# Kernel optimization log

Measured on AMD Instinct MI355X. Metric: run time of the kernel, lower is better.

## Reference

```python
import jax, jax.numpy as jnp
import numpy as np

GROUP = 128  # per-group quantization along the input dimension


def _quantize_int4(w):
    """Asymmetric INT4 per-group quantization. w: [out, in] -> (q, scale, zero).
    q: int32 in [0,15], shape [out, in//GROUP, GROUP]; scale/zero: [out, in//GROUP]."""
    o, i = w.shape
    wg = w.reshape(o, i // GROUP, GROUP)
    mn = wg.min(axis=-1)
    mx = wg.max(axis=-1)
    scale = (mx - mn) / 15.0
    scale = jnp.where(scale == 0, jnp.float32(1.0), scale)
    zero = jnp.clip(jnp.round(-mn / scale), 0.0, 15.0)
    q = jnp.clip(jnp.round(wg / scale[..., None]) + zero[..., None], 0.0, 15.0).astype(jnp.int32)
    return q, scale.astype(jnp.float32), zero.astype(jnp.float32)


def _dequant(q, s, z):
    """(q - zero) * scale, regrouped back to [out, in]."""
    w = (q.astype(jnp.float32) - z[..., None]) * s[..., None]
    return w.reshape(q.shape[0], -1)


def setup_inputs() -> dict:
    key = jax.random.key(0)
    ks = jax.random.split(key, 5)
    B, D_IN, D_H, D_OUT = 512, 2048, 8192, 2048
    x = jax.random.normal(ks[0], (B, D_IN), dtype=jnp.float32)
    w1 = jax.random.normal(ks[1], (D_H, D_IN), dtype=jnp.float32) * 0.02
    b1 = jax.random.normal(ks[2], (D_H,), dtype=jnp.float32) * 0.01
    w2 = jax.random.normal(ks[3], (D_OUT, D_H), dtype=jnp.float32) * 0.02
    b2 = jax.random.normal(ks[4], (D_OUT,), dtype=jnp.float32) * 0.01
    q1, s1, z1 = _quantize_int4(w1)
    q2, s2, z2 = _quantize_int4(w2)
    return {"x": x, "q1": q1, "s1": s1, "z1": z1, "b1": b1,
            "q2": q2, "s2": s2, "z2": z2, "b2": b2}


def reference(x, q1, s1, z1, b1, q2, s2, z2, b2):
    # Layer 1: INT4 dequant + Linear + ReLU (fused in the native kernel)
    w1 = _dequant(q1, s1, z1)              # [D_H, D_IN]
    h = jax.nn.relu(x @ w1.T + b1)         # [B, D_H]
    # Layer 2: INT4 dequant + Linear (no activation)
    w2 = _dequant(q2, s2, z2)              # [D_OUT, D_H]
    return h @ w2.T + b2                   # [B, D_OUT]
```

## Files before the change

### kernel.cpp

```cpp
#include <hip/hip_runtime.h>
#include <stdint.h>

typedef unsigned short u16;
typedef __attribute__((ext_vector_type(8))) short bf16x8;
typedef __attribute__((ext_vector_type(8))) unsigned short u16x8;
typedef __attribute__((ext_vector_type(4))) float f32x4;
typedef __attribute__((ext_vector_type(4))) int i32x4;

__device__ __forceinline__ u16 f2bf(float f) {
  uint32_t u = __builtin_bit_cast(uint32_t, f);
  u += 0x7fffu + ((u >> 16) & 1u);
  return (u16)(u >> 16);
}

#define GLD16(g, l)                                                         \
  __builtin_amdgcn_global_load_lds(                                         \
      (const __attribute__((address_space(1))) void*)(g),                   \
      (__attribute__((address_space(3))) void*)(l), 16, 0, 0)


__global__ __launch_bounds__(256) void cvt_f32_bf16(const float* __restrict__ src,
                                                    u16* __restrict__ dst, int n8) {
  int t = blockIdx.x * 256 + threadIdx.x;
  if (t >= n8) return;
  f32x4 a = ((const f32x4*)src)[2 * t];
  f32x4 b = ((const f32x4*)src)[2 * t + 1];
  u16x8 o;
  o[0] = f2bf(a[0]); o[1] = f2bf(a[1]); o[2] = f2bf(a[2]); o[3] = f2bf(a[3]);
  o[4] = f2bf(b[0]); o[5] = f2bf(b[1]); o[6] = f2bf(b[2]); o[7] = f2bf(b[3]);
  ((u16x8*)dst)[t] = o;
}

__global__ __launch_bounds__(256) void dequant_w2x(const int* __restrict__ qa,
                                                   const float* __restrict__ sa,
                                                   const float* __restrict__ za,
                                                   u16* __restrict__ wa,
                                                   const int* __restrict__ qb,
                                                   const float* __restrict__ sb,
                                                   const float* __restrict__ zb,
                                                   u16* __restrict__ wb, int n8) {
  int t = blockIdx.x * 256 + threadIdx.x;
  if (t >= n8) return;
  const int* q = blockIdx.z ? qb : qa;
  const float* s = blockIdx.z ? sb : sa;
  const float* z = blockIdx.z ? zb : za;
  u16* w = blockIdx.z ? wb : wa;
  int g = t >> 4;
  float sc = s[g];
  float zp = z[g];
  i32x4 a = ((const i32x4*)q)[2 * t];
  i32x4 b = ((const i32x4*)q)[2 * t + 1];
  u16x8 o;
  o[0] = f2bf(((float)a[0] - zp) * sc);
  o[1] = f2bf(((float)a[1] - zp) * sc);
  o[2] = f2bf(((float)a[2] - zp) * sc);
  o[3] = f2bf(((float)a[3] - zp) * sc);
  o[4] = f2bf(((float)b[0] - zp) * sc);
  o[5] = f2bf(((float)b[1] - zp) * sc);
  o[6] = f2bf(((float)b[2] - zp) * sc);
  o[7] = f2bf(((float)b[3] - zp) * sc);
  ((u16x8*)w)[t] = o;
}

__global__ __launch_bounds__(256) void bias_init(float* __restrict__ out,
                                                 const float* __restrict__ b,
                                                 int N, int n4) {
  int t = blockIdx.x * 256 + threadIdx.x;
  if (t >= n4) return;
  int idx = t * 4;
  int n = idx & (N - 1);
  *(f32x4*)(out + idx) = *(const f32x4*)(b + n);
}

template <bool RELU, bool OUT_BF16, bool ATOMIC>
__global__ __launch_bounds__(256) void gemm_bt(const u16* __restrict__ A,
                                               const u16* __restrict__ Bm,
                                               const float* __restrict__ bias,
                                               void* __restrict__ Cout,
                                               int M, int N, int K, int kChunk) {
  __shared__ u16 As[2][128 * 64];
  __shared__ u16 Bs[2][128 * 64];
  const int tid = threadIdx.x;
  const int wave = tid >> 6;
  const int lane = tid & 63;
  const int m0 = blockIdx.y << 7;
  const int n0 = blockIdx.x << 7;
  const int kStart = blockIdx.z * kChunk;
  const int srow = lane >> 3;
  const int schunk = (((lane & 7) ^ (srow & 7)) << 3);
  const int wm = (wave >> 1) << 6;
  const int wn = (wave & 1) << 6;
  const int quad = lane >> 4;
  const int l15 = lane & 15;
  const int x7 = lane & 7;
  const int c0 = ((quad ^ x7) << 3);
  const int c1 = (((4 | quad) ^ x7) << 3);

  const u16* Ab = A + (size_t)(m0 + 32 * wave + srow) * K + kStart + schunk;
  const u16* Bb = Bm + (size_t)(n0 + 32 * wave + srow) * K + kStart + schunk;
  const int ldsW = (32 * wave) * 64;
  const size_t rs8 = (size_t)8 * K;
  const int nT = kChunk >> 6;

  f32x4 acc[4][4];
#pragma unroll
  for (int i = 0; i < 4; i++)
#pragma unroll
    for (int j = 0; j < 4; j++) acc[i][j] = (f32x4){0.f, 0.f, 0.f, 0.f};

#define STAGE(bi_, t_)                                          \
  do {                                                          \
    const int ko_ = (t_) << 6;                                  \
    GLD16(Ab + ko_,           &As[bi_][ldsW]);                  \
    GLD16(Ab + ko_ + rs8,     &As[bi_][ldsW + 512]);            \
    GLD16(Ab + ko_ + 2 * rs8, &As[bi_][ldsW + 1024]);           \
    GLD16(Ab + ko_ + 3 * rs8, &As[bi_][ldsW + 1536]);           \
    GLD16(Bb + ko_,           &Bs[bi_][ldsW]);                  \
    GLD16(Bb + ko_ + rs8,     &Bs[bi_][ldsW + 512]);            \
    GLD16(Bb + ko_ + 2 * rs8, &Bs[bi_][ldsW + 1024]);           \
    GLD16(Bb + ko_ + 3 * rs8, &Bs[bi_][ldsW + 1536]);           \
  } while (0)

  bf16x8 af0[4], bf0[4], af1[4], bf1[4];
#define LOADFRAGS(bi_)                                                          \
  do {                                                                          \
    _Pragma("unroll") for (int i = 0; i < 4; i++)                               \
        af0[i] = *(const bf16x8*)&As[bi_][(wm + i * 16 + l15) * 64 + c0];       \
    _Pragma("unroll") for (int j = 0; j < 4; j++)                               \
        bf0[j] = *(const bf16x8*)&Bs[bi_][(wn + j * 16 + l15) * 64 + c0];       \
    _Pragma("unroll") for (int i = 0; i < 4; i++)                               \
        af1[i] = *(const bf16x8*)&As[bi_][(wm + i * 16 + l15) * 64 + c1];       \
    _Pragma("unroll") for (int j = 0; j < 4; j++)                               \
        bf1[j] = *(const bf16x8*)&Bs[bi_][(wn + j * 16 + l15) * 64 + c1];       \
  } while (0)

#define MFMA_S0()                                                               \
  do {                                                                          \
    _Pragma("unroll") for (int i = 0; i < 4; i++)                               \
        _Pragma("unroll") for (int j = 0; j < 4; j++)                           \
            acc[i][j] = __builtin_amdgcn_mfma_f32_16x16x32_bf16(                \
                af0[i], bf0[j], acc[i][j], 0, 0, 0);                            \
  } while (0)

#define MFMA_S1()                                                               \
  do {                                                                          \
    _Pragma("unroll") for (int i = 0; i < 4; i++)                               \
        _Pragma("unroll") for (int j = 0; j < 4; j++)                           \
            acc[i][j] = __builtin_amdgcn_mfma_f32_16x16x32_bf16(                \
                af1[i], bf1[j], acc[i][j], 0, 0, 0);                            \
  } while (0)

  STAGE(0, 0);
  STAGE(1, 1);

  int bi = 0;
  for (int t = 0; t < nT - 2; ++t) {
    asm volatile("s_waitcnt vmcnt(8)" ::: "memory");
    __builtin_amdgcn_s_barrier();
    LOADFRAGS(bi);
    asm volatile("s_waitcnt lgkmcnt(8)" ::: "memory");
    __builtin_amdgcn_sched_barrier(0);
    MFMA_S0();
    asm volatile("s_waitcnt lgkmcnt(0)" ::: "memory");
    __builtin_amdgcn_sched_barrier(0);
    __builtin_amdgcn_s_barrier();
    STAGE(bi, t + 2);
    MFMA_S1();
    bi ^= 1;
  }
  asm volatile("s_waitcnt vmcnt(8)" ::: "memory");
  __builtin_amdgcn_s_barrier();
  LOADFRAGS(bi);
  asm volatile("s_waitcnt lgkmcnt(8)" ::: "memory");
  __builtin_amdgcn_sched_barrier(0);
  MFMA_S0();
  asm volatile("s_waitcnt lgkmcnt(0)" ::: "memory");
  __builtin_amdgcn_sched_barrier(0);
  MFMA_S1();
  bi ^= 1;
  asm volatile("s_waitcnt vmcnt(0)" ::: "memory");
  __builtin_amdgcn_s_barrier();
  LOADFRAGS(bi);
  asm volatile("s_waitcnt lgkmcnt(8)" ::: "memory");
  __builtin_amdgcn_sched_barrier(0);
  MFMA_S0();
  asm volatile("s_waitcnt lgkmcnt(0)" ::: "memory");
  __builtin_amdgcn_sched_barrier(0);
  MFMA_S1();

#undef STAGE
#undef LOADFRAGS
#undef MFMA_S0
#undef MFMA_S1

#pragma unroll
  for (int i = 0; i < 4; i++) {
#pragma unroll
    for (int j = 0; j < 4; j++) {
      const int col = n0 + wn + j * 16 + l15;
      float bv = 0.f;
      if (!ATOMIC) bv = bias[col];
#pragma unroll
      for (int r = 0; r < 4; r++) {
        const int row = m0 + wm + i * 16 + quad * 4 + r;
        float v = acc[i][j][r];
        if (ATOMIC) {
          atomicAdd((float*)Cout + (size_t)row * N + col, v);
        } else {
          v += bv;
          if (RELU) v = v > 0.f ? v : 0.f;
          if (OUT_BF16)
            ((u16*)Cout)[(size_t)row * N + col] = f2bf(v);
          else
            ((float*)Cout)[(size_t)row * N + col] = v;
        }
      }
    }
  }
}


extern "C" void kernel_launch(void* const* d_in, const int* in_sizes, int n_in,
                              void* d_out, int out_size, void* d_ws, size_t ws_size,
                              hipStream_t stream) {
  const float* x  = (const float*)d_in[0];
  const int*   q1 = (const int*)d_in[1];
  const float* s1 = (const float*)d_in[2];
  const float* z1 = (const float*)d_in[3];
  const float* b1 = (const float*)d_in[4];
  const int*   q2 = (const int*)d_in[5];
  const float* s2 = (const float*)d_in[6];
  const float* z2 = (const float*)d_in[7];
  const float* b2 = (const float*)d_in[8];
  float* out = (float*)d_out;

  const int B = 512, D_IN = 2048, D_H = 8192, D_OUT = 2048;

  char* ws = (char*)d_ws;
  u16* xb  = (u16*)(ws);
  u16* w1b = (u16*)(ws + (size_t)2 * 1024 * 1024);
  u16* hb  = (u16*)(ws + (size_t)34 * 1024 * 1024);
  u16* w2b = (u16*)(ws + (size_t)42 * 1024 * 1024);

  cvt_f32_bf16<<<(B * D_IN / 8 + 255) / 256, 256, 0, stream>>>(x, xb, B * D_IN / 8);
  {
    const int n8 = D_H * D_IN / 8;
    dim3 gd((n8 + 255) / 256, 1, 2);
    dequant_w2x<<<gd, 256, 0, stream>>>(q1, s1, z1, w1b, q2, s2, z2, w2b, n8);
  }
  dim3 g1(D_H / 128, B / 128, 1);
  gemm_bt<true, true, false><<<g1, 256, 0, stream>>>(xb, w1b, b1, hb, B, D_H, D_IN, D_IN);
  bias_init<<<(B * D_OUT / 4 + 255) / 256, 256, 0, stream>>>(out, b2, D_OUT, B * D_OUT / 4);
  dim3 g2(D_OUT / 128, B / 128, 8);
  gemm_bt<false, false, true><<<g2, 256, 0, stream>>>(hb, w2b, nullptr, out, B, D_OUT, D_H, D_H / 8);
}
```

Measured before the change: 244.2 us.

## Fuse all stages into one persistent kernel with grid-wide barriers

Replaces the five separate launches (convert, dequant, GEMM1, bias init, split-K GEMM2) with a single persistent kernel of 256 blocks. Blocks do the elementwise stages with grid-stride loops, then synchronize through atomic-counter grid barriers before each GEMM phase. This removes launch gaps and inter-kernel idle time, but adds a memset plus spin-wait barriers. It also relies on all 256 blocks being co-resident, and GEMM2 has only one block per work item.

```diff
diff --git a/kernel.cpp b/kernel.cpp
--- a/kernel.cpp
+++ b/kernel.cpp
@@ -2,6 +2,7 @@
 #include <stdint.h>
 
 typedef unsigned short u16;
+typedef unsigned int u32;
 typedef __attribute__((ext_vector_type(8))) short bf16x8;
 typedef __attribute__((ext_vector_type(8))) unsigned short u16x8;
 typedef __attribute__((ext_vector_type(4))) float f32x4;
@@ -18,33 +19,21 @@
       (const __attribute__((address_space(1))) void*)(g),                   \
       (__attribute__((address_space(3))) void*)(l), 16, 0, 0)
 
-
-__global__ __launch_bounds__(256) void cvt_f32_bf16(const float* __restrict__ src,
-                                                    u16* __restrict__ dst, int n8) {
-  int t = blockIdx.x * 256 + threadIdx.x;
-  if (t >= n8) return;
-  f32x4 a = ((const f32x4*)src)[2 * t];
-  f32x4 b = ((const f32x4*)src)[2 * t + 1];
-  u16x8 o;
-  o[0] = f2bf(a[0]); o[1] = f2bf(a[1]); o[2] = f2bf(a[2]); o[3] = f2bf(a[3]);
-  o[4] = f2bf(b[0]); o[5] = f2bf(b[1]); o[6] = f2bf(b[2]); o[7] = f2bf(b[3]);
-  ((u16x8*)dst)[t] = o;
-}
-
-__global__ __launch_bounds__(256) void dequant_w2x(const int* __restrict__ qa,
-                                                   const float* __restrict__ sa,
-                                                   const float* __restrict__ za,
-                                                   u16* __restrict__ wa,
-                                                   const int* __restrict__ qb,
-                                                   const float* __restrict__ sb,
-                                                   const float* __restrict__ zb,
-                                                   u16* __restrict__ wb, int n8) {
-  int t = blockIdx.x * 256 + threadIdx.x;
-  if (t >= n8) return;
-  const int* q = blockIdx.z ? qb : qa;
-  const float* s = blockIdx.z ? sb : sa;
-  const float* z = blockIdx.z ? zb : za;
-  u16* w = blockIdx.z ? wb : wa;
+__device__ __forceinline__ void grid_barrier(u32* ctr, u32 nb) {
+  __syncthreads();
+  if (threadIdx.x == 0) {
+    __threadfence();
+    u32 old = atomicAdd(ctr, 1u);
+    if (old + 1u < nb) {
+      while (atomicAdd(ctr, 0u) < nb) __builtin_amdgcn_s_sleep(2);
+    }
+    __threadfence();
+  }
+  __syncthreads();
+}
+
+__device__ __forceinline__ void deq8(const int* __restrict__ q, const float* __restrict__ s,
+                                     const float* __restrict__ z, u16* __restrict__ w, int t) {
   int g = t >> 4;
   float sc = s[g];
   float zp = z[g];
@@ -62,30 +51,17 @@
   ((u16x8*)w)[t] = o;
 }
 
-__global__ __launch_bounds__(256) void bias_init(float* __restrict__ out,
-                                                 const float* __restrict__ b,
-                                                 int N, int n4) {
-  int t = blockIdx.x * 256 + threadIdx.x;
-  if (t >= n4) return;
-  int idx = t * 4;
-  int n = idx & (N - 1);
-  *(f32x4*)(out + idx) = *(const f32x4*)(b + n);
-}
-
 template <bool RELU, bool OUT_BF16, bool ATOMIC>
-__global__ __launch_bounds__(256) void gemm_bt(const u16* __restrict__ A,
-                                               const u16* __restrict__ Bm,
-                                               const float* __restrict__ bias,
-                                               void* __restrict__ Cout,
-                                               int M, int N, int K, int kChunk) {
-  __shared__ u16 As[2][128 * 64];
-  __shared__ u16 Bs[2][128 * 64];
+__device__ __forceinline__ void gemm_phase(const u16* __restrict__ A,
+                                           const u16* __restrict__ Bm,
+                                           const float* __restrict__ bias,
+                                           void* __restrict__ Cout,
+                                           int N, int K, int kChunk,
+                                           int m0, int n0, int kStart,
+                                           u16* As, u16* Bs) {
   const int tid = threadIdx.x;
   const int wave = tid >> 6;
   const int lane = tid & 63;
-  const int m0 = blockIdx.y << 7;
-  const int n0 = blockIdx.x << 7;
-  const int kStart = blockIdx.z * kChunk;
   const int srow = lane >> 3;
   const int schunk = (((lane & 7) ^ (srow & 7)) << 3);
   const int wm = (wave >> 1) << 6;
@@ -108,30 +84,30 @@
 #pragma unroll
     for (int j = 0; j < 4; j++) acc[i][j] = (f32x4){0.f, 0.f, 0.f, 0.f};
 
-#define STAGE(bi_, t_)                                          \
-  do {                                                          \
-    const int ko_ = (t_) << 6;                                  \
-    GLD16(Ab + ko_,           &As[bi_][ldsW]);                  \
-    GLD16(Ab + ko_ + rs8,     &As[bi_][ldsW + 512]);            \
-    GLD16(Ab + ko_ + 2 * rs8, &As[bi_][ldsW + 1024]);           \
-    GLD16(Ab + ko_ + 3 * rs8, &As[bi_][ldsW + 1536]);           \
-    GLD16(Bb + ko_,           &Bs[bi_][ldsW]);                  \
-    GLD16(Bb + ko_ + rs8,     &Bs[bi_][ldsW + 512]);            \
-    GLD16(Bb + ko_ + 2 * rs8, &Bs[bi_][ldsW + 1024]);           \
-    GLD16(Bb + ko_ + 3 * rs8, &Bs[bi_][ldsW + 1536]);           \
+#define STAGE(bi_, t_)                                                \
+  do {                                                                \
+    const int ko_ = (t_) << 6;                                        \
+    GLD16(Ab + ko_,           As + (bi_) * 8192 + ldsW);              \
+    GLD16(Ab + ko_ + rs8,     As + (bi_) * 8192 + ldsW + 512);        \
+    GLD16(Ab + ko_ + 2 * rs8, As + (bi_) * 8192 + ldsW + 1024);       \
+    GLD16(Ab + ko_ + 3 * rs8, As + (bi_) * 8192 + ldsW + 1536);       \
+    GLD16(Bb + ko_,           Bs + (bi_) * 8192 + ldsW);              \
+    GLD16(Bb + ko_ + rs8,     Bs + (bi_) * 8192 + ldsW + 512);        \
+    GLD16(Bb + ko_ + 2 * rs8, Bs + (bi_) * 8192 + ldsW + 1024);       \
+    GLD16(Bb + ko_ + 3 * rs8, Bs + (bi_) * 8192 + ldsW + 1536);       \
   } while (0)
 
   bf16x8 af0[4], bf0[4], af1[4], bf1[4];
-#define LOADFRAGS(bi_)                                                          \
-  do {                                                                          \
-    _Pragma("unroll") for (int i = 0; i < 4; i++)                               \
-        af0[i] = *(const bf16x8*)&As[bi_][(wm + i * 16 + l15) * 64 + c0];       \
-    _Pragma("unroll") for (int j = 0; j < 4; j++)                               \
-        bf0[j] = *(const bf16x8*)&Bs[bi_][(wn + j * 16 + l15) * 64 + c0];       \
-    _Pragma("unroll") for (int i = 0; i < 4; i++)                               \
-        af1[i] = *(const bf16x8*)&As[bi_][(wm + i * 16 + l15) * 64 + c1];       \
-    _Pragma("unroll") for (int j = 0; j < 4; j++)                               \
-        bf1[j] = *(const bf16x8*)&Bs[bi_][(wn + j * 16 + l15) * 64 + c1];       \
+#define LOADFRAGS(bi_)                                                               \
+  do {                                                                               \
+    _Pragma("unroll") for (int i = 0; i < 4; i++)                                    \
+        af0[i] = *(const bf16x8*)&As[(bi_) * 8192 + (wm + i * 16 + l15) * 64 + c0];  \
+    _Pragma("unroll") for (int j = 0; j < 4; j++)                                    \
+        bf0[j] = *(const bf16x8*)&Bs[(bi_) * 8192 + (wn + j * 16 + l15) * 64 + c0];  \
+    _Pragma("unroll") for (int i = 0; i < 4; i++)                                    \
+        af1[i] = *(const bf16x8*)&As[(bi_) * 8192 + (wm + i * 16 + l15) * 64 + c1];  \
+    _Pragma("unroll") for (int j = 0; j < 4; j++)                                    \
+        bf1[j] = *(const bf16x8*)&Bs[(bi_) * 8192 + (wn + j * 16 + l15) * 64 + c1];  \
   } while (0)
 
 #define MFMA_S0()                                                               \
@@ -219,6 +195,52 @@
   }
 }
 
+__global__ __launch_bounds__(256) void fused_all(
+    const float* __restrict__ x,
+    const int* __restrict__ q1, const float* __restrict__ s1, const float* __restrict__ z1,
+    const float* __restrict__ b1,
+    const int* __restrict__ q2, const float* __restrict__ s2, const float* __restrict__ z2,
+    const float* __restrict__ b2,
+    float* __restrict__ out,
+    u16* __restrict__ xb, u16* __restrict__ w1b, u16* __restrict__ hb, u16* __restrict__ w2b,
+    u32* bars) {
+  __shared__ u16 As[2 * 128 * 64];
+  __shared__ u16 Bs[2 * 128 * 64];
+
+  const int gstride = 256 * 256;
+  const int base = blockIdx.x * 256 + threadIdx.x;
+
+  for (int t = base; t < 131072; t += gstride) {
+    f32x4 a = ((const f32x4*)x)[2 * t];
+    f32x4 b = ((const f32x4*)x)[2 * t + 1];
+    u16x8 o;
+    o[0] = f2bf(a[0]); o[1] = f2bf(a[1]); o[2] = f2bf(a[2]); o[3] = f2bf(a[3]);
+    o[4] = f2bf(b[0]); o[5] = f2bf(b[1]); o[6] = f2bf(b[2]); o[7] = f2bf(b[3]);
+    ((u16x8*)xb)[t] = o;
+  }
+  for (int t = base; t < 2097152; t += gstride) deq8(q1, s1, z1, w1b, t);
+  for (int t = base; t < 2097152; t += gstride) deq8(q2, s2, z2, w2b, t);
+  for (int t = base; t < 262144; t += gstride) {
+    ((f32x4*)out)[t] = *(const f32x4*)(b2 + ((t * 4) & 2047));
+  }
+
+  grid_barrier(bars + 0, gridDim.x);
+
+  gemm_phase<true, true, false>(xb, w1b, b1, hb,
+                                8192, 2048, 2048,
+                                (blockIdx.x >> 6) << 7,
+                                (blockIdx.x & 63) << 7,
+                                0, As, Bs);
+
+  grid_barrier(bars + 1, gridDim.x);
+
+  gemm_phase<false, false, true>(hb, w2b, nullptr, out,
+                                 2048, 8192, 2048,
+                                 ((blockIdx.x >> 4) & 3) << 7,
+                                 (blockIdx.x & 15) << 7,
+                                 (blockIdx.x >> 6) << 11, As, Bs);
+}
+
 
 extern "C" void kernel_launch(void* const* d_in, const int* in_sizes, int n_in,
                               void* d_out, int out_size, void* d_ws, size_t ws_size,
@@ -234,23 +256,15 @@
   const float* b2 = (const float*)d_in[8];
   float* out = (float*)d_out;
 
-  const int B = 512, D_IN = 2048, D_H = 8192, D_OUT = 2048;
-
   char* ws = (char*)d_ws;
   u16* xb  = (u16*)(ws);
   u16* w1b = (u16*)(ws + (size_t)2 * 1024 * 1024);
   u16* hb  = (u16*)(ws + (size_t)34 * 1024 * 1024);
   u16* w2b = (u16*)(ws + (size_t)42 * 1024 * 1024);
-
-  cvt_f32_bf16<<<(B * D_IN / 8 + 255) / 256, 256, 0, stream>>>(x, xb, B * D_IN / 8);
-  {
-    const int n8 = D_H * D_IN / 8;
-    dim3 gd((n8 + 255) / 256, 1, 2);
-    dequant_w2x<<<gd, 256, 0, stream>>>(q1, s1, z1, w1b, q2, s2, z2, w2b, n8);
-  }
-  dim3 g1(D_H / 128, B / 128, 1);
-  gemm_bt<true, true, false><<<g1, 256, 0, stream>>>(xb, w1b, b1, hb, B, D_H, D_IN, D_IN);
-  bias_init<<<(B * D_OUT / 4 + 255) / 256, 256, 0, stream>>>(out, b2, D_OUT, B * D_OUT / 4);
-  dim3 g2(D_OUT / 128, B / 128, 8);
-  gemm_bt<false, false, true><<<g2, 256, 0, stream>>>(hb, w2b, nullptr, out, B, D_OUT, D_H, D_H / 8);
-}
+  u32* bars = (u32*)(ws + (size_t)74 * 1024 * 1024);
+
+  hipMemsetAsync(bars, 0, 2 * sizeof(u32), stream);
+
+  fused_all<<<256, 256, 0, stream>>>(x, q1, s1, z1, b1, q2, s2, z2, b2,
+                                     out, xb, w1b, hb, w2b, bars);
+}
```

Result: slower. 288.3 us (+18.1%).

## Fuse INT4 dequantization into GEMM B-tile staging, drop separate dequant pass

Applied to the files above, without the earlier changes.

Removes the standalone dequant kernel that wrote bf16 copies of both weight matrices. Each GEMM now loads the int32 quantized weights into registers, converts them with scale and zero to bf16, and writes them into swizzled LDS, interleaved with the MFMA pipeline. This avoids writing and then re-reading the bf16 weights in global memory. In exchange each tile reads int32 weights, twice the bytes of bf16, and adds conversion ALU work and register pressure. Since the 128-column weight tiles are re-dequantized by each of the 4 M-block rows, global weight traffic may not shrink much.

```diff
diff --git a/kernel.cpp b/kernel.cpp
--- a/kernel.cpp
+++ b/kernel.cpp
@@ -2,6 +2,7 @@
 #include <stdint.h>
 
 typedef unsigned short u16;
+typedef unsigned int u32;
 typedef __attribute__((ext_vector_type(8))) short bf16x8;
 typedef __attribute__((ext_vector_type(8))) unsigned short u16x8;
 typedef __attribute__((ext_vector_type(4))) float f32x4;
@@ -31,37 +32,6 @@
   ((u16x8*)dst)[t] = o;
 }
 
-__global__ __launch_bounds__(256) void dequant_w2x(const int* __restrict__ qa,
-                                                   const float* __restrict__ sa,
-                                                   const float* __restrict__ za,
-                                                   u16* __restrict__ wa,
-                                                   const int* __restrict__ qb,
-                                                   const float* __restrict__ sb,
-                                                   const float* __restrict__ zb,
-                                                   u16* __restrict__ wb, int n8) {
-  int t = blockIdx.x * 256 + threadIdx.x;
-  if (t >= n8) return;
-  const int* q = blockIdx.z ? qb : qa;
-  const float* s = blockIdx.z ? sb : sa;
-  const float* z = blockIdx.z ? zb : za;
-  u16* w = blockIdx.z ? wb : wa;
-  int g = t >> 4;
-  float sc = s[g];
-  float zp = z[g];
-  i32x4 a = ((const i32x4*)q)[2 * t];
-  i32x4 b = ((const i32x4*)q)[2 * t + 1];
-  u16x8 o;
-  o[0] = f2bf(((float)a[0] - zp) * sc);
-  o[1] = f2bf(((float)a[1] - zp) * sc);
-  o[2] = f2bf(((float)a[2] - zp) * sc);
-  o[3] = f2bf(((float)a[3] - zp) * sc);
-  o[4] = f2bf(((float)b[0] - zp) * sc);
-  o[5] = f2bf(((float)b[1] - zp) * sc);
-  o[6] = f2bf(((float)b[2] - zp) * sc);
-  o[7] = f2bf(((float)b[3] - zp) * sc);
-  ((u16x8*)w)[t] = o;
-}
-
 __global__ __launch_bounds__(256) void bias_init(float* __restrict__ out,
                                                  const float* __restrict__ b,
                                                  int N, int n4) {
@@ -73,11 +43,13 @@
 }
 
 template <bool RELU, bool OUT_BF16, bool ATOMIC>
-__global__ __launch_bounds__(256) void gemm_bt(const u16* __restrict__ A,
-                                               const u16* __restrict__ Bm,
-                                               const float* __restrict__ bias,
-                                               void* __restrict__ Cout,
-                                               int M, int N, int K, int kChunk) {
+__global__ __launch_bounds__(256, 2) void gemm_dq(const u16* __restrict__ A,
+                                                  const int* __restrict__ Q,
+                                                  const float* __restrict__ S,
+                                                  const float* __restrict__ Z,
+                                                  const float* __restrict__ bias,
+                                                  void* __restrict__ Cout,
+                                                  int N, int K, int kChunk) {
   __shared__ u16 As[2][128 * 64];
   __shared__ u16 Bs[2][128 * 64];
   const int tid = threadIdx.x;
@@ -86,8 +58,20 @@
   const int m0 = blockIdx.y << 7;
   const int n0 = blockIdx.x << 7;
   const int kStart = blockIdx.z * kChunk;
+
   const int srow = lane >> 3;
   const int schunk = (((lane & 7) ^ (srow & 7)) << 3);
+  const u16* Ab = A + (size_t)(m0 + 32 * wave + srow) * K + kStart + schunk;
+  const size_t rs8 = (size_t)8 * K;
+
+  const int br = lane >> 1;
+  const int hf = lane & 1;
+  const int brow = n0 + 32 * wave + br;
+  const int* Qb = Q + (size_t)brow * K + kStart + hf * 32;
+  const int nG = K >> 7;
+  const float* Sb = S + (size_t)brow * nG + (kStart >> 7);
+  const float* Zb = Z + (size_t)brow * nG + (kStart >> 7);
+
   const int wm = (wave >> 1) << 6;
   const int wn = (wave & 1) << 6;
   const int quad = lane >> 4;
@@ -96,10 +80,7 @@
   const int c0 = ((quad ^ x7) << 3);
   const int c1 = (((4 | quad) ^ x7) << 3);
 
-  const u16* Ab = A + (size_t)(m0 + 32 * wave + srow) * K + kStart + schunk;
-  const u16* Bb = Bm + (size_t)(n0 + 32 * wave + srow) * K + kStart + schunk;
   const int ldsW = (32 * wave) * 64;
-  const size_t rs8 = (size_t)8 * K;
   const int nT = kChunk >> 6;
 
   f32x4 acc[4][4];
@@ -108,17 +89,34 @@
 #pragma unroll
     for (int j = 0; j < 4; j++) acc[i][j] = (f32x4){0.f, 0.f, 0.f, 0.f};
 
-#define STAGE(bi_, t_)                                          \
-  do {                                                          \
-    const int ko_ = (t_) << 6;                                  \
-    GLD16(Ab + ko_,           &As[bi_][ldsW]);                  \
-    GLD16(Ab + ko_ + rs8,     &As[bi_][ldsW + 512]);            \
-    GLD16(Ab + ko_ + 2 * rs8, &As[bi_][ldsW + 1024]);           \
-    GLD16(Ab + ko_ + 3 * rs8, &As[bi_][ldsW + 1536]);           \
-    GLD16(Bb + ko_,           &Bs[bi_][ldsW]);                  \
-    GLD16(Bb + ko_ + rs8,     &Bs[bi_][ldsW + 512]);            \
-    GLD16(Bb + ko_ + 2 * rs8, &Bs[bi_][ldsW + 1024]);           \
-    GLD16(Bb + ko_ + 3 * rs8, &Bs[bi_][ldsW + 1536]);           \
+  i32x4 rA[8], rB[8];
+  float scA, zpA, scB, zpB;
+
+#define ISSUE(bi_, t_, rb_, sc_, zp_)                                 \
+  do {                                                                \
+    const int ko_ = (t_) << 6;                                        \
+    GLD16(Ab + ko_,           &As[bi_][ldsW]);                        \
+    GLD16(Ab + ko_ + rs8,     &As[bi_][ldsW + 512]);                  \
+    GLD16(Ab + ko_ + 2 * rs8, &As[bi_][ldsW + 1024]);                 \
+    GLD16(Ab + ko_ + 3 * rs8, &As[bi_][ldsW + 1536]);                 \
+    const i32x4* qp_ = (const i32x4*)(Qb + ko_);                      \
+    _Pragma("unroll") for (int j = 0; j < 8; j++) rb_[j] = qp_[j];    \
+    sc_ = Sb[(t_) >> 1];                                              \
+    zp_ = Zb[(t_) >> 1];                                              \
+  } while (0)
+
+#define CVTW(bi_, rb_, sc_, zp_)                                      \
+  do {                                                                \
+    u16* wp_ = &Bs[bi_][(32 * wave + br) * 64];                       \
+    _Pragma("unroll") for (int c = 0; c < 4; c++) {                   \
+      u16x8 o_;                                                       \
+      _Pragma("unroll") for (int e = 0; e < 4; e++) {                 \
+        o_[e]     = f2bf(((float)rb_[2 * c][e]     - (zp_)) * (sc_)); \
+        o_[e + 4] = f2bf(((float)rb_[2 * c + 1][e] - (zp_)) * (sc_)); \
+      }                                                               \
+      const int slot_ = ((hf * 4 + c) ^ (br & 7));                    \
+      *(u16x8*)(wp_ + slot_ * 8) = o_;                                \
+    }                                                                 \
   } while (0)
 
   bf16x8 af0[4], bf0[4], af1[4], bf1[4];
@@ -150,45 +148,57 @@
                 af1[i], bf1[j], acc[i][j], 0, 0, 0);                            \
   } while (0)
 
-  STAGE(0, 0);
-  STAGE(1, 1);
-
-  int bi = 0;
-  for (int t = 0; t < nT - 2; ++t) {
-    asm volatile("s_waitcnt vmcnt(8)" ::: "memory");
-    __builtin_amdgcn_s_barrier();
-    LOADFRAGS(bi);
+  ISSUE(0, 0, rA, scA, zpA);
+  ISSUE(1, 1, rB, scB, zpB);
+  asm volatile("s_waitcnt vmcnt(14)" ::: "memory");
+  CVTW(0, rA, scA, zpA);
+  asm volatile("s_waitcnt lgkmcnt(0)" ::: "memory");
+  __builtin_amdgcn_s_barrier();
+
+  for (int t = 0; t < nT; t += 2) {
+    LOADFRAGS(0);
     asm volatile("s_waitcnt lgkmcnt(8)" ::: "memory");
     __builtin_amdgcn_sched_barrier(0);
     MFMA_S0();
     asm volatile("s_waitcnt lgkmcnt(0)" ::: "memory");
     __builtin_amdgcn_sched_barrier(0);
     __builtin_amdgcn_s_barrier();
-    STAGE(bi, t + 2);
+    if (t + 2 < nT) ISSUE(0, t + 2, rA, scA, zpA);
     MFMA_S1();
-    bi ^= 1;
+    if (t + 2 < nT)
+      asm volatile("s_waitcnt vmcnt(14)" ::: "memory");
+    else
+      asm volatile("s_waitcnt vmcnt(0)" ::: "memory");
+    __builtin_amdgcn_sched_barrier(0);
+    CVTW(1, rB, scB, zpB);
+    asm volatile("s_waitcnt lgkmcnt(0)" ::: "memory");
+    __builtin_amdgcn_s_barrier();
+
+    LOADFRAGS(1);
+    asm volatile("s_waitcnt lgkmcnt(8)" ::: "memory");
+    __builtin_amdgcn_sched_barrier(0);
+    MFMA_S0();
+    asm volatile("s_waitcnt lgkmcnt(0)" ::: "memory");
+    __builtin_amdgcn_sched_barrier(0);
+    if (t + 2 >= nT) {
+      MFMA_S1();
+      break;
+    }
+    __builtin_amdgcn_s_barrier();
+    if (t + 3 < nT) ISSUE(1, t + 3, rB, scB, zpB);
+    MFMA_S1();
+    if (t + 3 < nT)
+      asm volatile("s_waitcnt vmcnt(14)" ::: "memory");
+    else
+      asm volatile("s_waitcnt vmcnt(0)" ::: "memory");
+    __builtin_amdgcn_sched_barrier(0);
+    CVTW(0, rA, scA, zpA);
+    asm volatile("s_waitcnt lgkmcnt(0)" ::: "memory");
+    __builtin_amdgcn_s_barrier();
   }
-  asm volatile("s_waitcnt vmcnt(8)" ::: "memory");
-  __builtin_amdgcn_s_barrier();
-  LOADFRAGS(bi);
-  asm volatile("s_waitcnt lgkmcnt(8)" ::: "memory");
-  __builtin_amdgcn_sched_barrier(0);
-  MFMA_S0();
-  asm volatile("s_waitcnt lgkmcnt(0)" ::: "memory");
-  __builtin_amdgcn_sched_barrier(0);
-  MFMA_S1();
-  bi ^= 1;
-  asm volatile("s_waitcnt vmcnt(0)" ::: "memory");
-  __builtin_amdgcn_s_barrier();
-  LOADFRAGS(bi);
-  asm volatile("s_waitcnt lgkmcnt(8)" ::: "memory");
-  __builtin_amdgcn_sched_barrier(0);
-  MFMA_S0();
-  asm volatile("s_waitcnt lgkmcnt(0)" ::: "memory");
-  __builtin_amdgcn_sched_barrier(0);
-  MFMA_S1();
-
-#undef STAGE
+
+#undef ISSUE
+#undef CVTW
 #undef LOADFRAGS
 #undef MFMA_S0
 #undef MFMA_S1
@@ -237,20 +247,15 @@
   const int B = 512, D_IN = 2048, D_H = 8192, D_OUT = 2048;
 
   char* ws = (char*)d_ws;
-  u16* xb  = (u16*)(ws);
-  u16* w1b = (u16*)(ws + (size_t)2 * 1024 * 1024);
-  u16* hb  = (u16*)(ws + (size_t)34 * 1024 * 1024);
-  u16* w2b = (u16*)(ws + (size_t)42 * 1024 * 1024);
+  u16* xb = (u16*)(ws);
+  u16* hb = (u16*)(ws + (size_t)2 * 1024 * 1024);
 
   cvt_f32_bf16<<<(B * D_IN / 8 + 255) / 256, 256, 0, stream>>>(x, xb, B * D_IN / 8);
-  {
-    const int n8 = D_H * D_IN / 8;
-    dim3 gd((n8 + 255) / 256, 1, 2);
-    dequant_w2x<<<gd, 256, 0, stream>>>(q1, s1, z1, w1b, q2, s2, z2, w2b, n8);
-  }
   dim3 g1(D_H / 128, B / 128, 1);
-  gemm_bt<true, true, false><<<g1, 256, 0, stream>>>(xb, w1b, b1, hb, B, D_H, D_IN, D_IN);
+  gemm_dq<true, true, false><<<g1, 256, 0, stream>>>(xb, q1, s1, z1, b1, hb,
+                                                     D_H, D_IN, D_IN);
   bias_init<<<(B * D_OUT / 4 + 255) / 256, 256, 0, stream>>>(out, b2, D_OUT, B * D_OUT / 4);
   dim3 g2(D_OUT / 128, B / 128, 8);
-  gemm_bt<false, false, true><<<g2, 256, 0, stream>>>(hb, w2b, nullptr, out, B, D_OUT, D_H, D_H / 8);
-}
+  gemm_dq<false, false, true><<<g2, 256, 0, stream>>>(hb, q2, s2, z2, nullptr, out,
+                                                      D_OUT, D_H, D_H / 8);
+}
```

Result: slower. 348.2 us (+42.6%).
